# Performance work log

Measured on AMD Instinct MI355X. Metric: run time of the kernel, lower is better.

## Reference

```python
import jax, jax.numpy as jnp
import numpy as np

B, N, K, D = 4, 20000, 16, 128


def setup_inputs() -> dict:
    key = jax.random.key(0)
    k1, k2, k3, k4, k5, k6 = jax.random.split(key, 6)
    node_embeddings = jax.random.normal(k1, (B, N, D), dtype=jnp.float32)
    knn_indices = jax.random.randint(k2, (B, N, K), 0, N, dtype=jnp.int32)
    # MLP params: Linear(3D -> D), GELU, Linear(D -> D)
    s1 = 1.0 / np.sqrt(3 * D)
    s2 = 1.0 / np.sqrt(D)
    W1 = jax.random.uniform(k3, (3 * D, D), dtype=jnp.float32, minval=-s1, maxval=s1)
    b1 = jax.random.uniform(k4, (D,), dtype=jnp.float32, minval=-s1, maxval=s1)
    W2 = jax.random.uniform(k5, (D, D), dtype=jnp.float32, minval=-s2, maxval=s2)
    b2 = jax.random.uniform(k6, (D,), dtype=jnp.float32, minval=-s2, maxval=s2)
    return {"node_embeddings": node_embeddings, "knn_indices": knn_indices,
            "W1": W1, "b1": b1, "W2": W2, "b2": b2}


def reference(node_embeddings, knn_indices, W1, b1, W2, b2):
    # gather neighbors: [B, N, K, D]
    neighbors = jnp.take_along_axis(node_embeddings[:, None, :, :],  # [B,1,N,D]
                                    knn_indices[:, :, :, None].astype(jnp.int32),
                                    axis=2)
    neighbor_mean = neighbors.mean(axis=2)  # [B, N, D]
    feats = jnp.concatenate([node_embeddings, neighbor_mean,
                             node_embeddings - neighbor_mean], axis=-1)  # [B,N,3D]
    h = jax.nn.gelu(feats @ W1 + b1, approximate=False)
    update = h @ W2 + b2
    return node_embeddings + update
```

## Files before the change

kernel.cpp:

```cpp
#include <hip/hip_runtime.h>

#define NB      20000
#define BATCH   4
#define KNN     16
#define DD      128
#define MW      136
#define BMF     64
#define NSLOTF  157

#define PT_ROWS   16
#define PT_TPB    1250
#define GB_BYTES  32768
#define XB_BYTES  8192
#define MB_BYTES  4096
#define HB_BYTES  4096
#define PT_LDS    (GB_BYTES + 2*XB_BYTES + MB_BYTES + HB_BYTES)

#if defined(__has_builtin)
#if __has_builtin(__builtin_amdgcn_cvt_pk_f32_fp8)
#define FP8_DEC_BUILTIN 1
#endif
#endif

typedef __attribute__((ext_vector_type(8))) short          bf16x8;
typedef __attribute__((ext_vector_type(4))) float          f32x4;
typedef __attribute__((ext_vector_type(2))) float          f32x2;
typedef __attribute__((ext_vector_type(4))) int            i32x4;
typedef __attribute__((ext_vector_type(2))) int            i32x2;
typedef __attribute__((ext_vector_type(4))) unsigned short u16x4;
typedef __attribute__((ext_vector_type(8))) unsigned short u16x8;

__device__ __forceinline__ unsigned short f2bf(float f) {
    unsigned int u = __float_as_uint(f);
    u += 0x7fffu + ((u >> 16) & 1u);
    return (unsigned short)(u >> 16);
}
__device__ __forceinline__ float bf2f(unsigned short u) {
    return __uint_as_float((unsigned int)u << 16);
}
__device__ __forceinline__ float gelu_fast(float z) {
    float u = z * (0.7978845608028654f + 0.0356774081f * z * z);
    float e = __expf(-2.0f * u);
    return z * __builtin_amdgcn_rcpf(1.0f + e);
}
__device__ __forceinline__ void glds16(const void* g, void* l) {
    __builtin_amdgcn_global_load_lds(
        (const __attribute__((address_space(1))) void*)g,
        (__attribute__((address_space(3))) void*)l, 16, 0, 0);
}
__device__ __forceinline__ void bar_lgkm() {
    asm volatile("s_waitcnt lgkmcnt(0)" ::: "memory");
    __builtin_amdgcn_sched_barrier(0);
    __builtin_amdgcn_s_barrier();
}
__device__ __forceinline__ void bar_full() {
    asm volatile("s_waitcnt vmcnt(0) lgkmcnt(0)" ::: "memory");
    __builtin_amdgcn_sched_barrier(0);
    __builtin_amdgcn_s_barrier();
}
__device__ __forceinline__ unsigned int f32_to_e4m3(float x) {
    unsigned int u   = __float_as_uint(x);
    unsigned int sgn = (u >> 24) & 0x80u;
    float ax = fabsf(x);
    unsigned int em;
    if (ax < 0.015625f) {
        em = (unsigned int)rintf(ax * 512.0f);
    } else {
        unsigned int mag = __float_as_uint(fminf(ax, 448.0f));
        em = ((mag + 0x7FFFFu + ((mag >> 20) & 1u)) >> 20) - 0x3C0u;
    }
    return sgn | em;
}
__device__ __forceinline__ void acc4_fp8(unsigned int w, float* s) {
#if defined(FP8_DEC_BUILTIN)
    f32x2 lo = __builtin_amdgcn_cvt_pk_f32_fp8((int)w, false);
    f32x2 hi = __builtin_amdgcn_cvt_pk_f32_fp8((int)w, true);
    s[0] += lo[0]; s[1] += lo[1]; s[2] += hi[0]; s[3] += hi[1];
#else
    #pragma unroll
    for (int j = 0; j < 4; ++j) {
        unsigned int b  = (w >> (8 * j)) & 0xFFu;
        unsigned int em = b & 0x7Fu;
        float f  = __uint_as_float((em << 20) + 0x3C000000u);
        float fd = (float)em * 0.001953125f;
        f = (em < 8u) ? fd : f;
        f = __uint_as_float(__float_as_uint(f) | ((b & 0x80u) << 24));
        s[j] += f;
    }
#endif
}

__device__ __forceinline__ const bf16x8* wfrag(const void* W, int col, int ko) {
    return (const bf16x8*)((const char*)W + col * 256 + (ko ^ ((col & 7) << 4)));
}

template<bool DO_EMB>
__global__ __launch_bounds__(256) void nr_prep(
    const float* __restrict__ emb, const float* __restrict__ W1,
    const float* __restrict__ W2,
    unsigned char* __restrict__ embq, unsigned short* __restrict__ Wsw)
{
    int bid = blockIdx.x;
    if (DO_EMB && bid < 5000) {
        long long i = ((long long)bid * 256 + threadIdx.x) * 8;
        const float4* p = (const float4*)(emb + i);
        float4 a = p[0], b = p[1];
        unsigned int w0 = f32_to_e4m3(a.x) | (f32_to_e4m3(a.y) << 8) |
                          (f32_to_e4m3(a.z) << 16) | (f32_to_e4m3(a.w) << 24);
        unsigned int w1 = f32_to_e4m3(b.x) | (f32_to_e4m3(b.y) << 8) |
                          (f32_to_e4m3(b.z) << 16) | (f32_to_e4m3(b.w) << 24);
        i32x2 q; q[0] = (int)w0; q[1] = (int)w1;
        *(i32x2*)(embq + i) = q;
    } else {
        int tid = (bid - (DO_EMB ? 5000 : 0)) * 256 + threadIdx.x;
        int w   = tid >> 14;
        int r2  = tid & 16383;
        int col = r2 >> 7;
        int k   = r2 & 127;
        float v;
        if (w == 0)      v = W1[k * DD + col] + W1[(256 + k) * DD + col];
        else if (w == 1) v = W1[(128 + k) * DD + col] - W1[(256 + k) * DD + col];
        else             v = W2[k * DD + col];
        char* dst = (char*)Wsw + w * 32768 + col * 256 + ((k * 2) ^ ((col & 7) << 4));
        *(unsigned short*)dst = f2bf(v);
    }
}

__global__ __launch_bounds__(256, 2) void nr_persist(
    const float* __restrict__ emb, const unsigned char* __restrict__ embq,
    const int* __restrict__ knn, const unsigned short* __restrict__ Wsw,
    const float* __restrict__ b1, const float* __restrict__ b2,
    float* __restrict__ out)
{
    extern __shared__ char L[];
    char* GB  = L;
    char* XB0 = L + GB_BYTES;
    char* MB  = XB0 + 2 * XB_BYTES;
    char* HB  = MB + MB_BYTES;

    const int t     = threadIdx.x;
    const int xcd   = blockIdx.x & 7;
    const int bslot = blockIdx.x >> 3;
    const int batch = xcd >> 1;
    const int pair  = (xcd & 1) * 64 + bslot;
    const int wv    = t >> 6;
    const int ln    = t & 63;
    const int lrow  = ln & 15;
    const int lk    = ln >> 4;
    const int arow  = lrow;
    const int xsw   = (arow & 7) << 4;

    int   colj[2]; float b1v[2], b2v[2];
    #pragma unroll
    for (int j = 0; j < 2; ++j) {
        colj[j] = wv * 32 + j * 16 + lrow;
        b1v[j]  = b1[colj[j]];
        b2v[j]  = b2[colj[j]];
    }

    bf16x8 wA[4][2], wB[4][2], wC[4][2];
    #pragma unroll
    for (int ks = 0; ks < 4; ++ks)
        #pragma unroll
        for (int j = 0; j < 2; ++j) {
            int ko = ks * 64 + lk * 16;
            wA[ks][j] = *wfrag(Wsw, colj[j], ko);
            wB[ks][j] = *wfrag((const char*)Wsw + 32768, colj[j], ko);
            wC[ks][j] = *wfrag((const char*)Wsw + 65536, colj[j], ko);
        }

    const long long brow = (long long)batch * NB;
    const unsigned char* qb = embq + brow * DD;
    const int nt = (PT_TPB - pair + 127) >> 7;

    auto load_idx = [&](int n, int* iv) {
        const long long r0 = brow + (long long)(pair + n * 128) * PT_ROWS;
        const int* kp = knn + r0 * KNN + wv * 64 + (ln >> 3);
        #pragma unroll
        for (int c = 0; c < 8; ++c) iv[c] = kp[c * 8];
    };
    auto stage_g = [&](const int* iv) {
        #pragma unroll
        for (int c = 0; c < 8; ++c)
            glds16(qb + (long long)iv[c] * 128 + (ln & 7) * 16,
                   GB + (wv * 8 + c) * 1024);
    };
    auto stage_x = [&](int n) {
        const long long r0 = brow + (long long)(pair + n * 128) * PT_ROWS;
        char* xb = XB0 + (n & 1) * XB_BYTES;
        const char* gx = (const char*)emb + r0 * 512;
        #pragma unroll
        for (int ci = 0; ci < 2; ++ci) {
            int ch  = wv * 2 + ci;
            int row = ch * 2 + (ln >> 5);
            int cb  = (ln & 31) * 16;
            glds16(gx + (long long)row * 512 + (cb ^ ((row & 7) << 4)),
                   xb + ch * 1024);
        }
    };
    auto decode_mean = [&]() {
        int row = t >> 4;
        int e0  = (t & 15) * 8;
        float sm[8];
        #pragma unroll
        for (int e = 0; e < 8; ++e) sm[e] = 0.f;
        const char* gbase = GB + row * 2048 + e0;
        #pragma unroll
        for (int k = 0; k < KNN; ++k) {
            i32x2 v = *(const i32x2*)(gbase + k * 128);
            acc4_fp8((unsigned int)v[0], sm + 0);
            acc4_fp8((unsigned int)v[1], sm + 4);
        }
        u16x8 o;
        #pragma unroll
        for (int e = 0; e < 8; ++e) o[e] = f2bf(sm[e] * 0.0625f);
        *(u16x8*)(MB + row * 256 + ((e0 * 2) ^ ((row & 7) << 4))) = o;
    };

    int ivA[8], ivB[8];
    load_idx(0, ivA);
    stage_g(ivA);
    stage_x(0);
    if (nt > 1) load_idx(1, ivB);
    bar_full();

    for (int n = 0; n < nt; ++n) {
        const int p = n & 1;
        char* xb = XB0 + p * XB_BYTES;
        const long long r0 = brow + (long long)(pair + n * 128) * PT_ROWS;
        const bool have_next = (n + 1 < nt);

        decode_mean();
        bar_lgkm();

        if (have_next) {
            stage_g(ivB);
            stage_x(n + 1);
            if (n + 2 < nt) load_idx(n + 2, ivA);
        }

        bf16x8 xf[4], mf[4];
        #pragma unroll
        for (int ks = 0; ks < 4; ++ks) {
            int cb = ks * 128 + lk * 32;
            f32x4 a0 = *(const f32x4*)(xb + arow * 512 + ((cb)      ^ xsw));
            f32x4 a1 = *(const f32x4*)(xb + arow * 512 + ((cb + 16) ^ xsw));
            u16x8 xt;
            xt[0]=f2bf(a0[0]); xt[1]=f2bf(a0[1]); xt[2]=f2bf(a0[2]); xt[3]=f2bf(a0[3]);
            xt[4]=f2bf(a1[0]); xt[5]=f2bf(a1[1]); xt[6]=f2bf(a1[2]); xt[7]=f2bf(a1[3]);
            xf[ks] = *(bf16x8*)&xt;
            mf[ks] = *(const bf16x8*)(MB + arow * 256 + ((ks * 64 + lk * 16) ^ xsw));
        }

        f32x4 acc[2];
        acc[0] = (f32x4){0.f,0.f,0.f,0.f}; acc[1] = (f32x4){0.f,0.f,0.f,0.f};
        #pragma unroll
        for (int ks = 0; ks < 4; ++ks)
            #pragma unroll
            for (int j = 0; j < 2; ++j)
                acc[j] = __builtin_amdgcn_mfma_f32_16x16x32_bf16(xf[ks], wA[ks][j], acc[j], 0, 0, 0);
        #pragma unroll
        for (int ks = 0; ks < 4; ++ks)
            #pragma unroll
            for (int j = 0; j < 2; ++j)
                acc[j] = __builtin_amdgcn_mfma_f32_16x16x32_bf16(mf[ks], wB[ks][j], acc[j], 0, 0, 0);

        #pragma unroll
        for (int j = 0; j < 2; ++j)
            #pragma unroll
            for (int rr = 0; rr < 4; ++rr) {
                int row = lk * 4 + rr;
                *(unsigned short*)(HB + row * 256 + ((colj[j] * 2) ^ ((row & 7) << 4)))
                    = f2bf(gelu_fast(acc[j][rr] + b1v[j]));
            }
        bar_lgkm();

        bf16x8 hf[4];
        #pragma unroll
        for (int ks = 0; ks < 4; ++ks)
            hf[ks] = *(const bf16x8*)(HB + arow * 256 + ((ks * 64 + lk * 16) ^ xsw));
        f32x4 acc2[2];
        acc2[0] = (f32x4){0.f,0.f,0.f,0.f}; acc2[1] = (f32x4){0.f,0.f,0.f,0.f};
        #pragma unroll
        for (int ks = 0; ks < 4; ++ks)
            #pragma unroll
            for (int j = 0; j < 2; ++j)
                acc2[j] = __builtin_amdgcn_mfma_f32_16x16x32_bf16(hf[ks], wC[ks][j], acc2[j], 0, 0, 0);

        #pragma unroll
        for (int j = 0; j < 2; ++j)
            #pragma unroll
            for (int rr = 0; rr < 4; ++rr) {
                int row = lk * 4 + rr;
                *(unsigned short*)(MB + row * 256 + ((colj[j] * 2) ^ ((row & 7) << 4)))
                    = f2bf(acc2[j][rr] + b2v[j]);
            }
        bar_lgkm();

        #pragma unroll
        for (int i = 0; i < 2; ++i) {
            int flat = i * 1024 + t * 4;
            int row  = flat >> 7;
            int col  = flat & 127;
            int sw   = (row & 7) << 4;
            u16x4 uv = *(const u16x4*)(MB + row * 256 + ((col * 2) ^ sw));
            f32x4 rv = *(const f32x4*)(xb + row * 512 + ((col * 4) ^ sw));
            f32x4 ov;
            ov[0] = rv[0] + bf2f(uv[0]); ov[1] = rv[1] + bf2f(uv[1]);
            ov[2] = rv[2] + bf2f(uv[2]); ov[3] = rv[3] + bf2f(uv[3]);
            *(f32x4*)(out + r0 * 128 + flat) = ov;
        }

        if (have_next) {
            #pragma unroll
            for (int c = 0; c < 8; ++c) ivB[c] = ivA[c];
        }
        bar_full();
    }
}

__global__ __launch_bounds__(256, 3) void nr_fused_f32(
    const float* __restrict__ emb, const int* __restrict__ knn,
    const unsigned short* __restrict__ Wsw,
    const float* __restrict__ b1, const float* __restrict__ b2,
    float* __restrict__ out)
{
    extern __shared__ char ldsraw[];
    float*          ldsxF = (float*)ldsraw;
    unsigned short* ldsm  = (unsigned short*)(ldsraw + BMF * DD * 4);

    const int t     = threadIdx.x;
    const int xcd   = blockIdx.x & 7;
    const int slot  = blockIdx.x >> 3;
    const int batch = xcd >> 1;
    const int bib   = (xcd & 1) * NSLOTF + slot;
    const int mend  = batch * NB + NB;
    int m_base = batch * NB + bib * BMF;
    if (m_base + BMF > mend) m_base = mend - BMF;

    {
        const int node_local = t >> 2;
        const int dpart      = t & 3;
        const int m  = m_base + node_local;

        const f32x4* xp = (const f32x4*)(emb + (long long)m * DD + dpart * 32);
        float* xrow = ldsxF + node_local * DD + dpart * 32;
        #pragma unroll
        for (int j = 0; j < 8; ++j) {
            f32x4 v = xp[j];
            *(f32x4*)(xrow + j*4) = v;
        }
        int idx[KNN];
        const i32x4* kp4 = (const i32x4*)(knn + (long long)m * KNN);
        #pragma unroll
        for (int q = 0; q < 4; ++q) {
            i32x4 v = __builtin_nontemporal_load(kp4 + q);
            idx[4*q+0]=v[0]; idx[4*q+1]=v[1]; idx[4*q+2]=v[2]; idx[4*q+3]=v[3];
        }
        float sm[32];
        #pragma unroll
        for (int e = 0; e < 32; ++e) sm[e] = 0.f;
        const long long bbase = (long long)batch * NB * DD + dpart * 32;
        #pragma unroll 4
        for (int k = 0; k < KNN; ++k) {
            const f32x4* np = (const f32x4*)(emb + bbase + (long long)idx[k] * DD);
            #pragma unroll
            for (int j = 0; j < 8; ++j) {
                f32x4 v = np[j];
                sm[j*4+0]+=v[0]; sm[j*4+1]+=v[1]; sm[j*4+2]+=v[2]; sm[j*4+3]+=v[3];
            }
        }
        unsigned short* mrow = ldsm + node_local * MW + dpart * 32;
        #pragma unroll
        for (int j = 0; j < 8; ++j) {
            u16x4 pm;
            #pragma unroll
            for (int e = 0; e < 4; ++e) pm[e] = f2bf(sm[j*4+e] * 0.0625f);
            *(u16x4*)(mrow + j*4) = pm;
        }
    }
    __syncthreads();

    const int wave = t >> 6;
    const int lane = t & 63;
    const int lrow = lane & 15;
    const int lk   = lane >> 4;
    const int Arow = wave * 16 + lrow;

    bf16x8 xf[4], mf[4];
    {
        const float* xr = ldsxF + Arow * DD + lk * 8;
        const unsigned short* mr = ldsm + Arow * MW + lk * 8;
        #pragma unroll
        for (int ks = 0; ks < 4; ++ks) {
            f32x4 a0 = *(const f32x4*)(xr + ks * 32);
            f32x4 a1 = *(const f32x4*)(xr + ks * 32 + 4);
            u16x8 xt;
            xt[0]=f2bf(a0[0]); xt[1]=f2bf(a0[1]); xt[2]=f2bf(a0[2]); xt[3]=f2bf(a0[3]);
            xt[4]=f2bf(a1[0]); xt[5]=f2bf(a1[1]); xt[6]=f2bf(a1[2]); xt[7]=f2bf(a1[3]);
            xf[ks] = *(bf16x8*)&xt;
            mf[ks] = *(const bf16x8*)(mr + ks * 32);
        }
    }

    f32x4 acc[8];
    #pragma unroll
    for (int f = 0; f < 8; ++f) acc[f] = (f32x4){0.f, 0.f, 0.f, 0.f};
    #pragma unroll
    for (int ks = 0; ks < 4; ++ks)
        #pragma unroll
        for (int f = 0; f < 8; ++f) {
            bf16x8 bw = *wfrag(Wsw, f * 16 + lrow, ks * 64 + lk * 16);
            acc[f] = __builtin_amdgcn_mfma_f32_16x16x32_bf16(xf[ks], bw, acc[f], 0, 0, 0);
        }
    #pragma unroll
    for (int ks = 0; ks < 4; ++ks)
        #pragma unroll
        for (int f = 0; f < 8; ++f) {
            bf16x8 bw = *wfrag((const char*)Wsw + 32768, f * 16 + lrow, ks * 64 + lk * 16);
            acc[f] = __builtin_amdgcn_mfma_f32_16x16x32_bf16(mf[ks], bw, acc[f], 0, 0, 0);
        }
    __syncthreads();

    #pragma unroll
    for (int f = 0; f < 8; ++f) {
        int col = f * 16 + lrow;
        float bb = b1[col];
        #pragma unroll
        for (int rr = 0; rr < 4; ++rr) {
            int row = wave * 16 + lk * 4 + rr;
            ldsm[row * MW + col] = f2bf(gelu_fast(acc[f][rr] + bb));
        }
    }
    __syncthreads();

    f32x4 acc2[8];
    #pragma unroll
    for (int f = 0; f < 8; ++f) acc2[f] = (f32x4){0.f, 0.f, 0.f, 0.f};
    {
        const unsigned short* abase = ldsm + Arow * MW + lk * 8;
        #pragma unroll
        for (int ks = 0; ks < 4; ++ks) {
            bf16x8 af = *(const bf16x8*)(abase + ks * 32);
            #pragma unroll
            for (int f = 0; f < 8; ++f) {
                bf16x8 bw = *wfrag((const char*)Wsw + 65536, f * 16 + lrow, ks * 64 + lk * 16);
                acc2[f] = __builtin_amdgcn_mfma_f32_16x16x32_bf16(af, bw, acc2[f], 0, 0, 0);
            }
        }
    }

    #pragma unroll
    for (int f = 0; f < 8; ++f) {
        int col = f * 16 + lrow;
        float bb = b2[col];
        #pragma unroll
        for (int rr = 0; rr < 4; ++rr) {
            int row = wave * 16 + lk * 4 + rr;
            float xv = ldsxF[row * DD + col];
            out[(long long)(m_base + row) * DD + col] = acc2[f][rr] + bb + xv;
        }
    }
}

extern "C" void kernel_launch(void* const* d_in, const int* in_sizes, int n_in,
                              void* d_out, int out_size, void* d_ws, size_t ws_size,
                              hipStream_t stream) {
    const float* emb = (const float*)d_in[0];
    const int*   knn = (const int*)  d_in[1];
    const float* W1  = (const float*)d_in[2];
    const float* b1  = (const float*)d_in[3];
    const float* W2  = (const float*)d_in[4];
    const float* b2  = (const float*)d_in[5];
    float* out = (float*)d_out;

    unsigned short* Wsw  = (unsigned short*)d_ws;
    unsigned char*  embq = (unsigned char*)(Wsw + 49152);

    const size_t NEED   = (size_t)98304 + 10240000;
    const size_t LDSB_F = (size_t)BMF * DD * 4 + (size_t)BMF * MW * 2;

    if (ws_size >= NEED) {
        nr_prep<true><<<5192, 256, 0, stream>>>(emb, W1, W2, embq, Wsw);
        nr_persist<<<512, 256, PT_LDS, stream>>>(
            emb, embq, knn, Wsw, b1, b2, out);
    } else {
        nr_prep<false><<<192, 256, 0, stream>>>(emb, W1, W2, nullptr, Wsw);
        nr_fused_f32<<<8 * NSLOTF, 256, LDSB_F, stream>>>(
            emb, knn, Wsw, b1, b2, out);
    }
}
```

Before: 52.73 us.

## Halve persistent tile to 8 rows and double resident blocks per CU

Result: slower. 159.3 us (+202.1%).

```diff
diff --git a/kernel.cpp b/kernel.cpp
--- a/kernel.cpp
+++ b/kernel.cpp
@@ -8,12 +8,12 @@
 #define BMF     64
 #define NSLOTF  157
 
-#define PT_ROWS   16
-#define PT_TPB    1250
-#define GB_BYTES  32768
-#define XB_BYTES  8192
-#define MB_BYTES  4096
-#define HB_BYTES  4096
+#define PT_ROWS   8
+#define PT_TPB    2500
+#define GB_BYTES  16384
+#define XB_BYTES  4096
+#define MB_BYTES  2048
+#define HB_BYTES  2048
 #define PT_LDS    (GB_BYTES + 2*XB_BYTES + MB_BYTES + HB_BYTES)
 
 #if defined(__has_builtin)
@@ -126,7 +126,7 @@
     }
 }
 
-__global__ __launch_bounds__(256, 2) void nr_persist(
+__global__ __launch_bounds__(256, 4) void nr_persist(
     const float* __restrict__ emb, const unsigned char* __restrict__ embq,
     const int* __restrict__ knn, const unsigned short* __restrict__ Wsw,
     const float* __restrict__ b1, const float* __restrict__ b2,
@@ -142,13 +142,13 @@
     const int xcd   = blockIdx.x & 7;
     const int bslot = blockIdx.x >> 3;
     const int batch = xcd >> 1;
-    const int pair  = (xcd & 1) * 64 + bslot;
+    const int pair  = (xcd & 1) * 128 + bslot;
     const int wv    = t >> 6;
     const int ln    = t & 63;
     const int lrow  = ln & 15;
     const int lk    = ln >> 4;
-    const int arow  = lrow;
-    const int xsw   = (arow & 7) << 4;
+    const int arc   = lrow & 7;
+    const int xsw   = arc << 4;
 
     int   colj[2]; float b1v[2], b2v[2];
     #pragma unroll
@@ -171,53 +171,48 @@
 
     const long long brow = (long long)batch * NB;
     const unsigned char* qb = embq + brow * DD;
-    const int nt = (PT_TPB - pair + 127) >> 7;
+    const int nt = (PT_TPB - pair + 255) >> 8;
 
     auto load_idx = [&](int n, int* iv) {
-        const long long r0 = brow + (long long)(pair + n * 128) * PT_ROWS;
-        const int* kp = knn + r0 * KNN + wv * 64 + (ln >> 3);
-        #pragma unroll
-        for (int c = 0; c < 8; ++c) iv[c] = kp[c * 8];
+        const long long r0 = brow + (long long)(pair + n * 256) * PT_ROWS;
+        const int* kp = knn + r0 * KNN + wv * 32 + (ln >> 3);
+        #pragma unroll
+        for (int c = 0; c < 4; ++c) iv[c] = kp[c * 8];
     };
     auto stage_g = [&](const int* iv) {
         #pragma unroll
-        for (int c = 0; c < 8; ++c)
+        for (int c = 0; c < 4; ++c)
             glds16(qb + (long long)iv[c] * 128 + (ln & 7) * 16,
-                   GB + (wv * 8 + c) * 1024);
+                   GB + (wv * 4 + c) * 1024);
     };
     auto stage_x = [&](int n) {
-        const long long r0 = brow + (long long)(pair + n * 128) * PT_ROWS;
+        const long long r0 = brow + (long long)(pair + n * 256) * PT_ROWS;
         char* xb = XB0 + (n & 1) * XB_BYTES;
         const char* gx = (const char*)emb + r0 * 512;
-        #pragma unroll
-        for (int ci = 0; ci < 2; ++ci) {
-            int ch  = wv * 2 + ci;
-            int row = ch * 2 + (ln >> 5);
-            int cb  = (ln & 31) * 16;
-            glds16(gx + (long long)row * 512 + (cb ^ ((row & 7) << 4)),
-                   xb + ch * 1024);
-        }
+        int row = wv * 2 + (ln >> 5);
+        int cb  = (ln & 31) * 16;
+        glds16(gx + (long long)row * 512 + (cb ^ ((row & 7) << 4)),
+               xb + wv * 1024);
     };
     auto decode_mean = [&]() {
-        int row = t >> 4;
-        int e0  = (t & 15) * 8;
-        float sm[8];
-        #pragma unroll
-        for (int e = 0; e < 8; ++e) sm[e] = 0.f;
+        int row = t >> 5;
+        int e0  = (t & 31) * 4;
+        float sm[4];
+        #pragma unroll
+        for (int e = 0; e < 4; ++e) sm[e] = 0.f;
         const char* gbase = GB + row * 2048 + e0;
         #pragma unroll
         for (int k = 0; k < KNN; ++k) {
-            i32x2 v = *(const i32x2*)(gbase + k * 128);
-            acc4_fp8((unsigned int)v[0], sm + 0);
-            acc4_fp8((unsigned int)v[1], sm + 4);
-        }
-        u16x8 o;
-        #pragma unroll
-        for (int e = 0; e < 8; ++e) o[e] = f2bf(sm[e] * 0.0625f);
-        *(u16x8*)(MB + row * 256 + ((e0 * 2) ^ ((row & 7) << 4))) = o;
+            int v = *(const int*)(gbase + k * 128);
+            acc4_fp8((unsigned int)v, sm);
+        }
+        u16x4 o;
+        #pragma unroll
+        for (int e = 0; e < 4; ++e) o[e] = f2bf(sm[e] * 0.0625f);
+        *(u16x4*)(MB + row * 256 + ((e0 * 2) ^ (row << 4))) = o;
     };
 
-    int ivA[8], ivB[8];
+    int ivA[4], ivB[4];
     load_idx(0, ivA);
     stage_g(ivA);
     stage_x(0);
@@ -227,7 +222,7 @@
     for (int n = 0; n < nt; ++n) {
         const int p = n & 1;
         char* xb = XB0 + p * XB_BYTES;
-        const long long r0 = brow + (long long)(pair + n * 128) * PT_ROWS;
+        const long long r0 = brow + (long long)(pair + n * 256) * PT_ROWS;
         const bool have_next = (n + 1 < nt);
 
         decode_mean();
@@ -243,13 +238,13 @@
         #pragma unroll
         for (int ks = 0; ks < 4; ++ks) {
             int cb = ks * 128 + lk * 32;
-            f32x4 a0 = *(const f32x4*)(xb + arow * 512 + ((cb)      ^ xsw));
-            f32x4 a1 = *(const f32x4*)(xb + arow * 512 + ((cb + 16) ^ xsw));
+            f32x4 a0 = *(const f32x4*)(xb + arc * 512 + ((cb)      ^ xsw));
+            f32x4 a1 = *(const f32x4*)(xb + arc * 512 + ((cb + 16) ^ xsw));
             u16x8 xt;
             xt[0]=f2bf(a0[0]); xt[1]=f2bf(a0[1]); xt[2]=f2bf(a0[2]); xt[3]=f2bf(a0[3]);
             xt[4]=f2bf(a1[0]); xt[5]=f2bf(a1[1]); xt[6]=f2bf(a1[2]); xt[7]=f2bf(a1[3]);
             xf[ks] = *(bf16x8*)&xt;
-            mf[ks] = *(const bf16x8*)(MB + arow * 256 + ((ks * 64 + lk * 16) ^ xsw));
+            mf[ks] = *(const bf16x8*)(MB + arc * 256 + ((ks * 64 + lk * 16) ^ xsw));
         }
 
         f32x4 acc[2];
@@ -265,20 +260,22 @@
             for (int j = 0; j < 2; ++j)
                 acc[j] = __builtin_amdgcn_mfma_f32_16x16x32_bf16(mf[ks], wB[ks][j], acc[j], 0, 0, 0);
 
-        #pragma unroll
-        for (int j = 0; j < 2; ++j)
-            #pragma unroll
-            for (int rr = 0; rr < 4; ++rr) {
-                int row = lk * 4 + rr;
-                *(unsigned short*)(HB + row * 256 + ((colj[j] * 2) ^ ((row & 7) << 4)))
-                    = f2bf(gelu_fast(acc[j][rr] + b1v[j]));
-            }
+        if (lk < 2) {
+            #pragma unroll
+            for (int j = 0; j < 2; ++j)
+                #pragma unroll
+                for (int rr = 0; rr < 4; ++rr) {
+                    int row = lk * 4 + rr;
+                    *(unsigned short*)(HB + row * 256 + ((colj[j] * 2) ^ (row << 4)))
+                        = f2bf(gelu_fast(acc[j][rr] + b1v[j]));
+                }
+        }
         bar_lgkm();
 
         bf16x8 hf[4];
         #pragma unroll
         for (int ks = 0; ks < 4; ++ks)
-            hf[ks] = *(const bf16x8*)(HB + arow * 256 + ((ks * 64 + lk * 16) ^ xsw));
+            hf[ks] = *(const bf16x8*)(HB + arc * 256 + ((ks * 64 + lk * 16) ^ xsw));
         f32x4 acc2[2];
         acc2[0] = (f32x4){0.f,0.f,0.f,0.f}; acc2[1] = (f32x4){0.f,0.f,0.f,0.f};
         #pragma unroll
@@ -287,22 +284,23 @@
             for (int j = 0; j < 2; ++j)
                 acc2[j] = __builtin_amdgcn_mfma_f32_16x16x32_bf16(hf[ks], wC[ks][j], acc2[j], 0, 0, 0);
 
-        #pragma unroll
-        for (int j = 0; j < 2; ++j)
-            #pragma unroll
-            for (int rr = 0; rr < 4; ++rr) {
-                int row = lk * 4 + rr;
-                *(unsigned short*)(MB + row * 256 + ((colj[j] * 2) ^ ((row & 7) << 4)))
-                    = f2bf(acc2[j][rr] + b2v[j]);
-            }
+        if (lk < 2) {
+            #pragma unroll
+            for (int j = 0; j < 2; ++j)
+                #pragma unroll
+                for (int rr = 0; rr < 4; ++rr) {
+                    int row = lk * 4 + rr;
+                    *(unsigned short*)(MB + row * 256 + ((colj[j] * 2) ^ (row << 4)))
+                        = f2bf(acc2[j][rr] + b2v[j]);
+                }
+        }
         bar_lgkm();
 
-        #pragma unroll
-        for (int i = 0; i < 2; ++i) {
-            int flat = i * 1024 + t * 4;
+        {
+            int flat = t * 4;
             int row  = flat >> 7;
             int col  = flat & 127;
-            int sw   = (row & 7) << 4;
+            int sw   = row << 4;
             u16x4 uv = *(const u16x4*)(MB + row * 256 + ((col * 2) ^ sw));
             f32x4 rv = *(const f32x4*)(xb + row * 512 + ((col * 4) ^ sw));
             f32x4 ov;
@@ -313,7 +311,7 @@
 
         if (have_next) {
             #pragma unroll
-            for (int c = 0; c < 8; ++c) ivB[c] = ivA[c];
+            for (int c = 0; c < 4; ++c) ivB[c] = ivA[c];
         }
         bar_full();
     }
@@ -482,7 +480,7 @@
 
     if (ws_size >= NEED) {
         nr_prep<true><<<5192, 256, 0, stream>>>(emb, W1, W2, embq, Wsw);
-        nr_persist<<<512, 256, PT_LDS, stream>>>(
+        nr_persist<<<1024, 256, PT_LDS, stream>>>(
             emb, embq, knn, Wsw, b1, b2, out);
     } else {
         nr_prep<false><<<192, 256, 0, stream>>>(emb, W1, W2, nullptr, Wsw);
```
